# Performance work log

Measured on AMD Instinct MI355X. Metric: run time of the kernel, lower is better.

Reference implementation:

```python
import jax, jax.numpy as jnp
import numpy as np

HID = 512      # LSTM hidden per direction (1024 // 2)
EMB = 768      # BERT hidden size
NUM_TAG = 9
B, S = 64, 512


def setup_inputs() -> dict:
    key = jax.random.key(0)
    ks = jax.random.split(key, 12)
    g = lambda k, sh, sc: (jax.random.normal(k, sh, jnp.float32) * sc)
    return {
        "x": jax.random.normal(ks[0], (B, S, EMB), jnp.float32),
        "mask": jnp.ones((B, S), jnp.int32),
        "target_tag": jax.random.randint(ks[1], (B, S), 0, NUM_TAG, jnp.int32),
        "w_ih_f": g(ks[2], (4 * HID, EMB), 0.02),
        "w_hh_f": g(ks[3], (4 * HID, HID), 0.02),
        "b_f": jnp.zeros((4 * HID,), jnp.float32),
        "w_ih_b": g(ks[4], (4 * HID, EMB), 0.02),
        "w_hh_b": g(ks[5], (4 * HID, HID), 0.02),
        "b_b": jnp.zeros((4 * HID,), jnp.float32),
        "w_out": g(ks[6], (NUM_TAG, 2 * HID), 0.02),
        "b_out": jnp.zeros((NUM_TAG,), jnp.float32),
        "start_trans": g(ks[7], (NUM_TAG,), 0.1),
        "end_trans": g(ks[8], (NUM_TAG,), 0.1),
        "trans": g(ks[9], (NUM_TAG, NUM_TAG), 0.1),
    }


def _lstm_dir(x, w_ih, w_hh, b, reverse):
    # x: [B,S,E] -> outputs [S,B,H]; PyTorch gate order i,f,g,o
    xp = jnp.einsum('bse,ge->sbg', x, w_ih) + b  # precompute input proj [S,B,4H]
    if reverse:
        xp = xp[::-1]
    Bq = x.shape[0]
    def step(carry, xt):
        h, c = carry
        pre = xt + h @ w_hh.T
        i, f, g_, o = jnp.split(pre, 4, axis=-1)
        c = jax.nn.sigmoid(f) * c + jax.nn.sigmoid(i) * jnp.tanh(g_)
        h = jax.nn.sigmoid(o) * jnp.tanh(c)
        return (h, c), h
    init = (jnp.zeros((Bq, HID), x.dtype), jnp.zeros((Bq, HID), x.dtype))
    _, hs = jax.lax.scan(step, init, xp)
    if reverse:
        hs = hs[::-1]
    return hs


def _crf_nll_token_mean(emis, tags, m, start_trans, end_trans, trans):
    # emis: [S,B,T] time-major; tags: [S,B] int; m: [S,B] float (mask)
    Sq, Bq, T = emis.shape
    bidx = jnp.arange(Bq)
    # ---- numerator: score of the gold path ----
    num = start_trans[tags[0]] + emis[0, bidx, tags[0]]
    trans_steps = trans[tags[:-1], tags[1:]]                                   # [S-1,B]
    emit_steps = jnp.take_along_axis(emis[1:], tags[1:, :, None], axis=2)[..., 0]
    num = num + ((trans_steps + emit_steps) * m[1:]).sum(0)
    last_idx = m.sum(0).astype(jnp.int32) - 1                                   # [B]
    num = num + end_trans[tags[last_idx, bidx]]
    # ---- denominator: forward algorithm (log-sum-exp recursion) ----
    alpha0 = start_trans + emis[0]                                              # [B,T]
    def step(alpha, em):
        emis_t, m_t = em
        nxt = jax.nn.logsumexp(alpha[:, :, None] + trans[None] + emis_t[:, None, :], axis=1)
        return jnp.where(m_t[:, None] > 0, nxt, alpha), None
    alpha, _ = jax.lax.scan(step, alpha0, (emis[1:], m[1:]))
    den = jax.nn.logsumexp(alpha + end_trans, axis=1)
    llh = num - den
    return -(llh.sum() / m.sum())  # reduction='token_mean', negated (model loss)


def reference(x, mask, target_tag, w_ih_f, w_hh_f, b_f, w_ih_b, w_hh_b, b_b,
              w_out, b_out, start_trans, end_trans, trans):
    hf = _lstm_dir(x, w_ih_f, w_hh_f, b_f, reverse=False)   # [S,B,H]
    hb = _lstm_dir(x, w_ih_b, w_hh_b, b_b, reverse=True)    # [S,B,H]
    h = jnp.concatenate([hf, hb], axis=-1)                  # [S,B,2H]
    emis = jnp.einsum('sbh,th->sbt', h, w_out) + b_out      # [S,B,T] (dropout=identity in eval)
    tags = target_tag.T                                     # [S,B]
    m = mask.T.astype(emis.dtype)                           # [S,B]
    return _crf_nll_token_mean(emis, tags, m, start_trans, end_trans, trans)
```

## Files before the change

kernel.cpp:

```cpp
#include <hip/hip_runtime.h>
#include <cstdint>
#include <cstddef>

#define SS   512
#define BB   64
#define EMBD 768
#define HIDN 512
#define G4   2048
#define NTAG 9

typedef __attribute__((ext_vector_type(8))) __bf16 bf16x8;
typedef __attribute__((ext_vector_type(4))) float  f32x4;
typedef unsigned long long u64;

union HCast { f32x4 f; bf16x8 h; };

__device__ inline void load_h16_bypass(const void* base, f32x4* f) {
  asm volatile(
    "global_load_dwordx4 %0, %16, off sc0 sc1\n\t"
    "global_load_dwordx4 %1, %16, off offset:64 sc0 sc1\n\t"
    "global_load_dwordx4 %2, %16, off offset:128 sc0 sc1\n\t"
    "global_load_dwordx4 %3, %16, off offset:192 sc0 sc1\n\t"
    "global_load_dwordx4 %4, %16, off offset:256 sc0 sc1\n\t"
    "global_load_dwordx4 %5, %16, off offset:320 sc0 sc1\n\t"
    "global_load_dwordx4 %6, %16, off offset:384 sc0 sc1\n\t"
    "global_load_dwordx4 %7, %16, off offset:448 sc0 sc1\n\t"
    "global_load_dwordx4 %8, %16, off offset:512 sc0 sc1\n\t"
    "global_load_dwordx4 %9, %16, off offset:576 sc0 sc1\n\t"
    "global_load_dwordx4 %10, %16, off offset:640 sc0 sc1\n\t"
    "global_load_dwordx4 %11, %16, off offset:704 sc0 sc1\n\t"
    "global_load_dwordx4 %12, %16, off offset:768 sc0 sc1\n\t"
    "global_load_dwordx4 %13, %16, off offset:832 sc0 sc1\n\t"
    "global_load_dwordx4 %14, %16, off offset:896 sc0 sc1\n\t"
    "global_load_dwordx4 %15, %16, off offset:960 sc0 sc1\n\t"
    "s_waitcnt vmcnt(0)"
    : "=&v"(f[0]), "=&v"(f[1]), "=&v"(f[2]), "=&v"(f[3]),
      "=&v"(f[4]), "=&v"(f[5]), "=&v"(f[6]), "=&v"(f[7]),
      "=&v"(f[8]), "=&v"(f[9]), "=&v"(f[10]), "=&v"(f[11]),
      "=&v"(f[12]), "=&v"(f[13]), "=&v"(f[14]), "=&v"(f[15])
    : "v"(base)
    : "memory");
}
__device__ inline void store_h8_bypass(void* p, u64 v) {
  asm volatile("global_store_dwordx2 %0, %1, off sc0 sc1" :: "v"(p), "v"(v) : "memory");
}
__device__ inline void store_i32_bypass(int* p, int v) {
  asm volatile("global_store_dword %0, %1, off sc0 sc1" :: "v"(p), "v"(v) : "memory");
}
__device__ inline int load_i32_bypass(const int* p) {
  int v;
  asm volatile("global_load_dword %0, %1, off sc0 sc1\n\ts_waitcnt vmcnt(0)"
               : "=v"(v) : "v"(p) : "memory");
  return v;
}

__global__ __launch_bounds__(256) void cvt_kernel(
    const float* __restrict__ src, __bf16* __restrict__ dst, int n8)
{
  int i = blockIdx.x * 256 + threadIdx.x;
  if (i >= n8) return;
  f32x4 a = *reinterpret_cast<const f32x4*>(src + 8 * (size_t)i);
  f32x4 b = *reinterpret_cast<const f32x4*>(src + 8 * (size_t)i + 4);
  bf16x8 o;
  o[0]=(__bf16)a[0]; o[1]=(__bf16)a[1]; o[2]=(__bf16)a[2]; o[3]=(__bf16)a[3];
  o[4]=(__bf16)b[0]; o[5]=(__bf16)b[1]; o[6]=(__bf16)b[2]; o[7]=(__bf16)b[3];
  *reinterpret_cast<bf16x8*>(dst + 8 * (size_t)i) = o;
}

__global__ __launch_bounds__(256, 2) void proj_kernel(
    const __bf16* __restrict__ xb, const __bf16* __restrict__ wfb,
    const __bf16* __restrict__ wbb, const float* __restrict__ bias_f,
    const float* __restrict__ bias_b, float* __restrict__ xp,
    int t0, int chunk)
{
  const int nb = blockIdx.x;
  const int tt = blockIdx.y;
  const int d  = blockIdx.z;
  const int s  = d ? (SS - 1 - (t0 + tt)) : (t0 + tt);
  const __bf16* __restrict__ wih = d ? wbb : wfb;
  const float*  __restrict__ bias = d ? bias_b : bias_f;

  const int t = threadIdx.x, wv = t >> 6, l = t & 63;
  const int quad = l >> 4, col = l & 15;

  const __bf16* brow[8];
  float bj[8];
  const int pbase = 128 * nb;
#pragma unroll
  for (int j = 0; j < 8; j++) {
    int p    = pbase + 16 * j + col;
    int gate = p & 3;
    int hc   = 16 * (p >> 6) + 4 * ((p >> 2) & 3) + ((p >> 4) & 3);
    int g    = gate * HIDN + hc;
    brow[j]  = wih + (size_t)g * EMBD + 8 * quad;
    bj[j]    = bias[g];
  }
  const __bf16* arow = xb + ((size_t)(16 * wv + col) * SS + s) * EMBD + 8 * quad;

  f32x4 acc[8];
#pragma unroll
  for (int j = 0; j < 8; j++) acc[j] = f32x4{0.f, 0.f, 0.f, 0.f};

  for (int kk = 0; kk < 24; kk++) {
    bf16x8 a = *reinterpret_cast<const bf16x8*>(arow + 32 * kk);
#pragma unroll
    for (int j = 0; j < 8; j++) {
      bf16x8 b = *reinterpret_cast<const bf16x8*>(brow[j] + 32 * kk);
      acc[j] = __builtin_amdgcn_mfma_f32_16x16x32_bf16(a, b, acc[j], 0, 0, 0);
    }
  }
  float* xpd = xp + (size_t)(d * chunk + tt) * (size_t)G4 * BB + 16 * wv + 4 * quad;
#pragma unroll
  for (int j = 0; j < 8; j++) {
    int p = pbase + 16 * j + col;
    f32x4 v = acc[j];
    v[0] += bj[j]; v[1] += bj[j]; v[2] += bj[j]; v[3] += bj[j];
    *reinterpret_cast<f32x4*>(xpd + (size_t)p * BB) = v;
  }
}

struct RecCtl {
  int prog[2][64];
  int pad[128];
};

struct RecParams {
  const float* xp;
  const float* whh_f;
  const float* whh_b;
  __bf16* hh;
  float*  cT;
  RecCtl* ctl;
  int     chunk;
};

__global__ __launch_bounds__(256, 1) void rec_kernel(RecParams p)
{
  const int wg   = blockIdx.x;
  const int d    = wg >> 5;
  const int sl   = wg & 31;
  const int t    = threadIdx.x;
  const int wv   = t >> 6;
  const int l    = t & 63;
  const int quad = l >> 4;
  const int col  = l & 15;
  const int hcl  = col >> 2;
  const int gate = col & 3;
  const int j4   = col & 3;

  const float* __restrict__ whh = d ? p.whh_b : p.whh_f;

  bf16x8 bfrag[4][16];
#pragma unroll
  for (int j = 0; j < 4; j++) {
    const int hcb = 16 * sl + 4 * hcl + j;
    const float* wr = whh + (size_t)(gate * HIDN + hcb) * HIDN + 8 * quad;
#pragma unroll
    for (int kk = 0; kk < 16; kk++) {
      f32x4 w0 = *reinterpret_cast<const f32x4*>(wr + 32 * kk);
      f32x4 w1 = *reinterpret_cast<const f32x4*>(wr + 32 * kk + 4);
      bf16x8 v;
      v[0] = (__bf16)w0[0]; v[1] = (__bf16)w0[1]; v[2] = (__bf16)w0[2]; v[3] = (__bf16)w0[3];
      v[4] = (__bf16)w1[0]; v[5] = (__bf16)w1[1]; v[6] = (__bf16)w1[2]; v[7] = (__bf16)w1[3];
      bfrag[j][kk] = v;
    }
  }

  const int bA = 16 * wv + col;
  const int bC = 16 * wv + 4 * quad + gate;
  const int hcs = 16 * sl + 4 * hcl;
  const size_t slotsz = (size_t)BB * HIDN;
  __bf16* hhd = p.hh + (size_t)d * (p.chunk + 1) * slotsz;
  const float* xpd = p.xp + (size_t)d * p.chunk * ((size_t)G4 * BB);

  float c[4];
#pragma unroll
  for (int j = 0; j < 4; j++)
    c[j] = p.cT[((size_t)d * HIDN + hcs + j) * BB + bC];

  f32x4 xpn[4];
#pragma unroll
  for (int j = 0; j < 4; j++)
    xpn[j] = *reinterpret_cast<const f32x4*>(
        xpd + (size_t)(64 * sl + 16 * j + col) * BB + 16 * wv + 4 * quad);

  int* prog = &p.ctl->prog[d][0];
  const int* myslot = prog + (l & 31);

  u64 hword = 0;
  for (int tt = 0; tt < p.chunk; tt++) {
    const char* hbase = (const char*)hhd + (size_t)tt * slotsz * 2
                      + (size_t)bA * (HIDN * 2) + quad * 16;
    f32x4 araw[16];
    load_h16_bypass(hbase, araw);
    bf16x8 afrag[16];
#pragma unroll
    for (int kk = 0; kk < 16; kk++) { HCast hc_; hc_.f = araw[kk]; afrag[kk] = hc_.h; }

    f32x4 acc[4][2];
#pragma unroll
    for (int j = 0; j < 4; j++) {
      acc[j][0] = xpn[j];
      acc[j][1] = f32x4{0.f, 0.f, 0.f, 0.f};
    }
#pragma unroll
    for (int kk = 0; kk < 16; kk += 2) {
#pragma unroll
      for (int j = 0; j < 4; j++) {
        acc[j][0] = __builtin_amdgcn_mfma_f32_16x16x32_bf16(afrag[kk],     bfrag[j][kk],     acc[j][0], 0, 0, 0);
        acc[j][1] = __builtin_amdgcn_mfma_f32_16x16x32_bf16(afrag[kk + 1], bfrag[j][kk + 1], acc[j][1], 0, 0, 0);
      }
    }

    hword = 0;
#pragma unroll
    for (int j = 0; j < 4; j++) {
      float v0 = acc[j][0][0] + acc[j][1][0];
      float v1 = acc[j][0][1] + acc[j][1][1];
      float v2 = acc[j][0][2] + acc[j][1][2];
      float v3 = acc[j][0][3] + acc[j][1][3];
      {
        float t0 = __shfl_xor(v1, 1); float t1 = __shfl_xor(v0, 1);
        float t2 = __shfl_xor(v3, 1); float t3 = __shfl_xor(v2, 1);
        if (j4 & 1) { v0 = t0; v2 = t2; } else { v1 = t1; v3 = t3; }
        float u0 = __shfl_xor(v2, 2); float u1 = __shfl_xor(v3, 2);
        float u2 = __shfl_xor(v0, 2); float u3 = __shfl_xor(v1, 2);
        if (j4 & 2) { v0 = u0; v1 = u1; } else { v2 = u2; v3 = u3; }
      }
      float ig = 1.f / (1.f + __expf(-v0));
      float fg = 1.f / (1.f + __expf(-v1));
      float gg = 1.f - 2.f / (__expf(2.f * v2) + 1.f);
      float og = 1.f / (1.f + __expf(-v3));
      c[j] = fg * c[j] + ig * gg;
      float hn = og * (1.f - 2.f / (__expf(2.f * c[j]) + 1.f));
      union { __bf16 b; unsigned short u; } cv; cv.b = (__bf16)hn;
      hword |= (u64)cv.u << (16 * j);
    }
    store_h8_bypass((char*)hhd + (size_t)(tt + 1) * slotsz * 2
                    + (size_t)bC * (HIDN * 2) + (size_t)hcs * 2, hword);

    if (tt + 1 < p.chunk) {
#pragma unroll
      for (int j = 0; j < 4; j++)
        xpn[j] = *reinterpret_cast<const f32x4*>(
            xpd + (size_t)(tt + 1) * ((size_t)G4 * BB)
            + (size_t)(64 * sl + 16 * j + col) * BB + 16 * wv + 4 * quad);
    }

    __builtin_amdgcn_s_waitcnt(0);
    __syncthreads();
    if (t == 0) store_i32_bypass(prog + sl, tt + 1);
    if (wv == 0) {
      const int tgt = tt + 1;
      while (true) {
        int v = load_i32_bypass(myslot);
        if (__ballot(v >= tgt) == ~0ull) break;
        __builtin_amdgcn_s_sleep(1);
      }
    }
    __syncthreads();
    __atomic_signal_fence(__ATOMIC_SEQ_CST);
  }

  store_h8_bypass((char*)hhd + (size_t)bC * (HIDN * 2) + (size_t)hcs * 2, hword);
#pragma unroll
  for (int j = 0; j < 4; j++)
    p.cT[((size_t)d * HIDN + hcs + j) * BB + bC] = c[j];
}

__global__ __launch_bounds__(256) void emis_kernel(
    const __bf16* __restrict__ hh, const float* __restrict__ w_out,
    float* __restrict__ emis_f, float* __restrict__ emis_b,
    int t0, int chunk)
{
  const int tt = blockIdx.x;
  const int d  = blockIdx.y;
  const int t  = threadIdx.x;
  const int b  = t & 63;
  const int grp = t >> 6;

  const __bf16* hp = hh + ((size_t)d * (chunk + 1) + tt + 1) * ((size_t)BB * HIDN)
                   + (size_t)b * HIDN;
  const float* w0 = w_out + (size_t)grp * (2 * HIDN) + d * HIDN;
  const float* w1 = w_out + (size_t)(grp + 4) * (2 * HIDN) + d * HIDN;
  const float* w2 = w_out + (size_t)8 * (2 * HIDN) + d * HIDN;

  float a0 = 0.f, a1 = 0.f, a2 = 0.f;
  for (int k = 0; k < HIDN; k += 8) {
    bf16x8 hv8 = *reinterpret_cast<const bf16x8*>(hp + k);
#pragma unroll
    for (int j = 0; j < 8; j++) {
      float hv = (float)hv8[j];
      a0 += hv * w0[k + j];
      a1 += hv * w1[k + j];
      a2 += hv * w2[k + j];
    }
  }
  const int sidx = (d == 0) ? (t0 + tt) : (SS - 1 - (t0 + tt));
  float* dst = d ? emis_b : emis_f;
  dst[((size_t)sidx * BB + b) * NTAG + grp]     = a0;
  dst[((size_t)sidx * BB + b) * NTAG + grp + 4] = a1;
  if (grp == 0) dst[((size_t)sidx * BB + b) * NTAG + 8] = a2;
}

__global__ __launch_bounds__(64) void crf_kernel(
    const float* __restrict__ emis_f, const float* __restrict__ emis_b,
    const float* __restrict__ b_out, const float* __restrict__ start_tr,
    const float* __restrict__ end_tr, const float* __restrict__ trans,
    const int* __restrict__ mask, const int* __restrict__ target,
    float* __restrict__ llh)
{
  const int b    = blockIdx.x;
  const int lane = threadIdx.x;

  auto E = [&](int s, int tg) -> float {
    size_t o = ((size_t)s * BB + b) * NTAG + tg;
    return emis_f[o] + emis_b[o] + b_out[tg];
  };

  float numpart = 0.f;
  int msum = 0;
  for (int s = lane; s < SS; s += 64) {
    int m = mask[b * SS + s];
    msum += m;
    if (s >= 1 && m > 0) {
      int tp = target[b * SS + s - 1];
      int tc = target[b * SS + s];
      numpart += trans[tp * NTAG + tc] + E(s, tc);
    }
  }
#pragma unroll
  for (int off = 32; off > 0; off >>= 1) {
    numpart += __shfl_down(numpart, off, 64);
    msum    += __shfl_down(msum, off, 64);
  }

  const int tc = lane;
  const bool act = (tc < NTAG);
  float trc[NTAG] = {0.f};
  float alpha = 0.f;
  if (act) {
#pragma unroll
    for (int i = 0; i < NTAG; i++) trc[i] = trans[i * NTAG + tc];
    alpha = start_tr[tc] + E(0, tc);
  }
  for (int s = 1; s < SS; s++) {
    float e = act ? E(s, tc) : 0.f;
    float av[NTAG];
    float mx = -3.0e30f;
#pragma unroll
    for (int i = 0; i < NTAG; i++) {
      av[i] = __shfl(alpha, i, 64) + trc[i];
      mx = fmaxf(mx, av[i]);
    }
    float sum = 0.f;
#pragma unroll
    for (int i = 0; i < NTAG; i++) sum += __expf(av[i] - mx);
    float nxt = mx + __logf(sum) + e;
    if (act && mask[b * SS + s] > 0) alpha = nxt;
  }
  float fv = act ? (alpha + end_tr[tc]) : -3.0e30f;
  float q[NTAG];
  float mx2 = -3.0e30f;
#pragma unroll
  for (int i = 0; i < NTAG; i++) {
    q[i] = __shfl(fv, i, 64);
    mx2 = fmaxf(mx2, q[i]);
  }
  float s2 = 0.f;
#pragma unroll
  for (int i = 0; i < NTAG; i++) s2 += __expf(q[i] - mx2);
  float den = mx2 + __logf(s2);

  if (lane == 0) {
    int last = msum - 1;
    int tg0 = target[b * SS + 0];
    int tgl = target[b * SS + last];
    float num = start_tr[tg0] + E(0, tg0) + numpart + end_tr[tgl];
    llh[b] = num - den;
  }
}

__global__ __launch_bounds__(256) void fin_kernel(
    const float* __restrict__ llh, const int* __restrict__ mask,
    float* __restrict__ out)
{
  __shared__ float sf[256];
  __shared__ int   si[256];
  const int t = threadIdx.x;
  float a = (t < BB) ? llh[t] : 0.f;
  int m = 0;
  for (int i = t; i < BB * SS; i += 256) m += mask[i];
  sf[t] = a; si[t] = m;
  __syncthreads();
  for (int o = 128; o > 0; o >>= 1) {
    if (t < o) { sf[t] += sf[t + o]; si[t] += si[t + o]; }
    __syncthreads();
  }
  if (t == 0) out[0] = -(sf[0] / (float)si[0]);
}

extern "C" void kernel_launch(void* const* d_in, const int* in_sizes, int n_in,
                              void* d_out, int out_size, void* d_ws, size_t ws_size,
                              hipStream_t stream)
{
  const float* x     = (const float*)d_in[0];
  const int*   mask  = (const int*)d_in[1];
  const int*   targ  = (const int*)d_in[2];
  const float* wih_f = (const float*)d_in[3];
  const float* whh_f = (const float*)d_in[4];
  const float* b_f   = (const float*)d_in[5];
  const float* wih_b = (const float*)d_in[6];
  const float* whh_b = (const float*)d_in[7];
  const float* b_b   = (const float*)d_in[8];
  const float* w_out = (const float*)d_in[9];
  const float* b_out = (const float*)d_in[10];
  const float* st    = (const float*)d_in[11];
  const float* et    = (const float*)d_in[12];
  const float* tr    = (const float*)d_in[13];
  float* out = (float*)d_out;

  const size_t nxb   = (size_t)BB * SS * EMBD;
  const size_t nwb   = (size_t)G4 * EMBD;
  const size_t ctl_i = sizeof(RecCtl) / 4;
  const size_t fixed_f = (size_t)2 * SS * BB * NTAG + 64 + (size_t)2 * HIDN * BB
                       + ctl_i + nxb / 2 + nwb;
  int chunk = 1;
  for (int c = SS; c >= 1; c >>= 1) {
    size_t need = fixed_f * 4 + (size_t)c * 2 * G4 * BB * 4
                + (size_t)2 * (c + 1) * BB * HIDN * 2;
    if (need <= ws_size) { chunk = c; break; }
  }

  float* fp = (float*)d_ws;
  float* emis_f = fp; fp += (size_t)SS * BB * NTAG;
  float* emis_b = fp; fp += (size_t)SS * BB * NTAG;
  float* llh    = fp; fp += 64;
  float* cT     = fp; fp += (size_t)2 * HIDN * BB;
  RecCtl* ctl   = (RecCtl*)fp; fp += ctl_i;
  __bf16* xb16  = (__bf16*)fp; fp += nxb / 2;
  __bf16* wfb16 = (__bf16*)fp; fp += nwb / 2;
  __bf16* wbb16 = (__bf16*)fp; fp += nwb / 2;
  float* xp     = fp; fp += (size_t)chunk * 2 * G4 * BB;
  __bf16* hh    = (__bf16*)fp;

  {
    int n8 = (int)(nxb / 8);
    cvt_kernel<<<dim3((n8 + 255) / 256), 256, 0, stream>>>(x, xb16, n8);
    int w8 = (int)(nwb / 8);
    cvt_kernel<<<dim3((w8 + 255) / 256), 256, 0, stream>>>(wih_f, wfb16, w8);
    cvt_kernel<<<dim3((w8 + 255) / 256), 256, 0, stream>>>(wih_b, wbb16, w8);
  }

  const size_t slotsz = (size_t)BB * HIDN;
  hipMemsetAsync(cT, 0, (size_t)2 * HIDN * BB * sizeof(float), stream);
  hipMemsetAsync(hh, 0, slotsz * sizeof(__bf16), stream);
  hipMemsetAsync(hh + (size_t)(chunk + 1) * slotsz, 0, slotsz * sizeof(__bf16), stream);

  const int nch = SS / chunk;
  for (int c = 0; c < nch; c++) {
    const int t0 = c * chunk;
    hipMemsetAsync(ctl, 0, sizeof(RecCtl), stream);
    proj_kernel<<<dim3(16, chunk, 2), 256, 0, stream>>>(
        xb16, wfb16, wbb16, b_f, b_b, xp, t0, chunk);
    RecParams rp{xp, whh_f, whh_b, hh, cT, ctl, chunk};
    void* ka[] = {&rp};
    hipLaunchCooperativeKernel(rec_kernel, dim3(64), dim3(256), ka, 0, stream);
    emis_kernel<<<dim3(chunk, 2), 256, 0, stream>>>(
        hh, w_out, emis_f, emis_b, t0, chunk);
  }
  crf_kernel<<<dim3(64), 64, 0, stream>>>(emis_f, emis_b, b_out, st, et, tr, mask, targ, llh);
  fin_kernel<<<dim3(1), 256, 0, stream>>>(llh, mask, out);
}
```

Before: 5.001 ms.

## Replace block barrier with per-wave flags and retile input projection via LDS

The recurrence kernel drops its per-step block-wide barrier and global spin. Each wave now publishes its own progress flag and polls the flags of the producer groups, running the MFMAs for each 256-byte chunk of h as soon as that chunk is ready, so the recurrent matmul overlaps with waiting. The projection kernel is retiled to stage x and W_ih tiles in shared memory, computing 64x256 outputs per block, and x is converted to a time-major bf16 layout so each timestep's rows are contiguous. These changes add finer-grained memory-ordering logic whose correctness depends on the flag store being ordered after the h store.

```diff
diff --git a/kernel.cpp b/kernel.cpp
--- a/kernel.cpp
+++ b/kernel.cpp
@@ -15,31 +15,22 @@
 
 union HCast { f32x4 f; bf16x8 h; };
 
-__device__ inline void load_h16_bypass(const void* base, f32x4* f) {
+__device__ inline void load_h4_bypass(const void* base, f32x4* f) {
   asm volatile(
-    "global_load_dwordx4 %0, %16, off sc0 sc1\n\t"
-    "global_load_dwordx4 %1, %16, off offset:64 sc0 sc1\n\t"
-    "global_load_dwordx4 %2, %16, off offset:128 sc0 sc1\n\t"
-    "global_load_dwordx4 %3, %16, off offset:192 sc0 sc1\n\t"
-    "global_load_dwordx4 %4, %16, off offset:256 sc0 sc1\n\t"
-    "global_load_dwordx4 %5, %16, off offset:320 sc0 sc1\n\t"
-    "global_load_dwordx4 %6, %16, off offset:384 sc0 sc1\n\t"
-    "global_load_dwordx4 %7, %16, off offset:448 sc0 sc1\n\t"
-    "global_load_dwordx4 %8, %16, off offset:512 sc0 sc1\n\t"
-    "global_load_dwordx4 %9, %16, off offset:576 sc0 sc1\n\t"
-    "global_load_dwordx4 %10, %16, off offset:640 sc0 sc1\n\t"
-    "global_load_dwordx4 %11, %16, off offset:704 sc0 sc1\n\t"
-    "global_load_dwordx4 %12, %16, off offset:768 sc0 sc1\n\t"
-    "global_load_dwordx4 %13, %16, off offset:832 sc0 sc1\n\t"
-    "global_load_dwordx4 %14, %16, off offset:896 sc0 sc1\n\t"
-    "global_load_dwordx4 %15, %16, off offset:960 sc0 sc1\n\t"
+    "global_load_dwordx4 %0, %4, off sc0 sc1\n\t"
+    "global_load_dwordx4 %1, %4, off offset:64 sc0 sc1\n\t"
+    "global_load_dwordx4 %2, %4, off offset:128 sc0 sc1\n\t"
+    "global_load_dwordx4 %3, %4, off offset:192 sc0 sc1\n\t"
     "s_waitcnt vmcnt(0)"
-    : "=&v"(f[0]), "=&v"(f[1]), "=&v"(f[2]), "=&v"(f[3]),
-      "=&v"(f[4]), "=&v"(f[5]), "=&v"(f[6]), "=&v"(f[7]),
-      "=&v"(f[8]), "=&v"(f[9]), "=&v"(f[10]), "=&v"(f[11]),
-      "=&v"(f[12]), "=&v"(f[13]), "=&v"(f[14]), "=&v"(f[15])
-    : "v"(base)
-    : "memory");
+    : "=&v"(f[0]), "=&v"(f[1]), "=&v"(f[2]), "=&v"(f[3])
+    : "v"(base) : "memory");
+}
+__device__ inline void load_flags2(const int* p, int& a, int& b) {
+  asm volatile(
+    "global_load_dword %0, %2, off sc0 sc1\n\t"
+    "global_load_dword %1, %2, off offset:256 sc0 sc1\n\t"
+    "s_waitcnt vmcnt(0)"
+    : "=&v"(a), "=&v"(b) : "v"(p) : "memory");
 }
 __device__ inline void store_h8_bypass(void* p, u64 v) {
   asm volatile("global_store_dwordx2 %0, %1, off sc0 sc1" :: "v"(p), "v"(v) : "memory");
@@ -47,11 +38,8 @@
 __device__ inline void store_i32_bypass(int* p, int v) {
   asm volatile("global_store_dword %0, %1, off sc0 sc1" :: "v"(p), "v"(v) : "memory");
 }
-__device__ inline int load_i32_bypass(const int* p) {
-  int v;
-  asm volatile("global_load_dword %0, %1, off sc0 sc1\n\ts_waitcnt vmcnt(0)"
-               : "=v"(v) : "v"(p) : "memory");
-  return v;
+__device__ inline void wait_vm0() {
+  asm volatile("s_waitcnt vmcnt(0)" ::: "memory");
 }
 
 __global__ __launch_bounds__(256) void cvt_kernel(
@@ -67,6 +55,23 @@
   *reinterpret_cast<bf16x8*>(dst + 8 * (size_t)i) = o;
 }
 
+__global__ __launch_bounds__(256) void cvt_x_kernel(
+    const float* __restrict__ x, __bf16* __restrict__ xb)
+{
+  int i = blockIdx.x * 256 + threadIdx.x;
+  int e8 = i % 96;
+  int r  = i / 96;
+  int b  = r & 63;
+  int s  = r >> 6;
+  const float* src = x + ((size_t)b * SS + s) * EMBD + e8 * 8;
+  f32x4 a = *reinterpret_cast<const f32x4*>(src);
+  f32x4 c = *reinterpret_cast<const f32x4*>(src + 4);
+  bf16x8 o;
+  o[0]=(__bf16)a[0]; o[1]=(__bf16)a[1]; o[2]=(__bf16)a[2]; o[3]=(__bf16)a[3];
+  o[4]=(__bf16)c[0]; o[5]=(__bf16)c[1]; o[6]=(__bf16)c[2]; o[7]=(__bf16)c[3];
+  *reinterpret_cast<bf16x8*>(xb + ((size_t)s * BB + b) * EMBD + e8 * 8) = o;
+}
+
 __global__ __launch_bounds__(256, 2) void proj_kernel(
     const __bf16* __restrict__ xb, const __bf16* __restrict__ wfb,
     const __bf16* __restrict__ wbb, const float* __restrict__ bias_f,
@@ -77,51 +82,85 @@
   const int tt = blockIdx.y;
   const int d  = blockIdx.z;
   const int s  = d ? (SS - 1 - (t0 + tt)) : (t0 + tt);
-  const __bf16* __restrict__ wih = d ? wbb : wfb;
+  const __bf16* __restrict__ wih  = d ? wbb : wfb;
   const float*  __restrict__ bias = d ? bias_b : bias_f;
 
-  const int t = threadIdx.x, wv = t >> 6, l = t & 63;
-  const int quad = l >> 4, col = l & 15;
-
-  const __bf16* brow[8];
-  float bj[8];
-  const int pbase = 128 * nb;
-#pragma unroll
-  for (int j = 0; j < 8; j++) {
-    int p    = pbase + 16 * j + col;
-    int gate = p & 3;
-    int hc   = 16 * (p >> 6) + 4 * ((p >> 2) & 3) + ((p >> 4) & 3);
-    int g    = gate * HIDN + hc;
-    brow[j]  = wih + (size_t)g * EMBD + 8 * quad;
-    bj[j]    = bias[g];
-  }
-  const __bf16* arow = xb + ((size_t)(16 * wv + col) * SS + s) * EMBD + 8 * quad;
-
-  f32x4 acc[8];
-#pragma unroll
-  for (int j = 0; j < 8; j++) acc[j] = f32x4{0.f, 0.f, 0.f, 0.f};
-
-  for (int kk = 0; kk < 24; kk++) {
-    bf16x8 a = *reinterpret_cast<const bf16x8*>(arow + 32 * kk);
-#pragma unroll
-    for (int j = 0; j < 8; j++) {
-      bf16x8 b = *reinterpret_cast<const bf16x8*>(brow[j] + 32 * kk);
-      acc[j] = __builtin_amdgcn_mfma_f32_16x16x32_bf16(a, b, acc[j], 0, 0, 0);
-    }
-  }
-  float* xpd = xp + (size_t)(d * chunk + tt) * (size_t)G4 * BB + 16 * wv + 4 * quad;
-#pragma unroll
-  for (int j = 0; j < 8; j++) {
-    int p = pbase + 16 * j + col;
-    f32x4 v = acc[j];
-    v[0] += bj[j]; v[1] += bj[j]; v[2] += bj[j]; v[3] += bj[j];
-    *reinterpret_cast<f32x4*>(xpd + (size_t)p * BB) = v;
-  }
+  __shared__ __bf16 Asm[64 * 80];
+  __shared__ __bf16 Bsm[256 * 80];
+
+  const int t    = threadIdx.x;
+  const int wv   = t >> 6;
+  const int l    = t & 63;
+  const int quad = l >> 4;
+  const int col  = l & 15;
+
+  float bj[4];
+#pragma unroll
+  for (int j = 0; j < 4; j++) {
+    int p = 256 * nb + 64 * wv + 16 * j + col;
+    int g = (p & 3) * HIDN + 16 * (p >> 6) + 4 * ((p >> 2) & 3) + ((p >> 4) & 3);
+    bj[j] = bias[g];
+  }
+
+  f32x4 acc[4][4];
+#pragma unroll
+  for (int i = 0; i < 4; i++)
+#pragma unroll
+    for (int j = 0; j < 4; j++) acc[i][j] = f32x4{0.f, 0.f, 0.f, 0.f};
+
+  const int r32 = t >> 3;
+  const int m8  = t & 7;
+  const __bf16* xrow_base = xb + (size_t)s * BB * EMBD;
+
+  for (int kc = 0; kc < 12; kc++) {
+    const int k0 = kc * 64;
+    __syncthreads();
+#pragma unroll
+    for (int rr = 0; rr < 2; rr++) {
+      int r = r32 + 32 * rr;
+      *reinterpret_cast<bf16x8*>(Asm + r * 80 + m8 * 8) =
+          *reinterpret_cast<const bf16x8*>(xrow_base + (size_t)r * EMBD + k0 + m8 * 8);
+    }
+#pragma unroll
+    for (int rr = 0; rr < 8; rr++) {
+      int r = r32 + 32 * rr;
+      int p = 256 * nb + r;
+      int g = (p & 3) * HIDN + 16 * (p >> 6) + 4 * ((p >> 2) & 3) + ((p >> 4) & 3);
+      *reinterpret_cast<bf16x8*>(Bsm + r * 80 + m8 * 8) =
+          *reinterpret_cast<const bf16x8*>(wih + (size_t)g * EMBD + k0 + m8 * 8);
+    }
+    __syncthreads();
+#pragma unroll
+    for (int kkk = 0; kkk < 2; kkk++) {
+      bf16x8 af[4], bf[4];
+#pragma unroll
+      for (int i = 0; i < 4; i++)
+        af[i] = *reinterpret_cast<const bf16x8*>(Asm + (16 * i + col) * 80 + kkk * 32 + quad * 8);
+#pragma unroll
+      for (int j = 0; j < 4; j++)
+        bf[j] = *reinterpret_cast<const bf16x8*>(Bsm + (64 * wv + 16 * j + col) * 80 + kkk * 32 + quad * 8);
+#pragma unroll
+      for (int i = 0; i < 4; i++)
+#pragma unroll
+        for (int j = 0; j < 4; j++)
+          acc[i][j] = __builtin_amdgcn_mfma_f32_16x16x32_bf16(af[i], bf[j], acc[i][j], 0, 0, 0);
+    }
+  }
+  float* xpd = xp + (size_t)(d * chunk + tt) * (size_t)G4 * BB;
+#pragma unroll
+  for (int i = 0; i < 4; i++)
+#pragma unroll
+    for (int j = 0; j < 4; j++) {
+      int p = 256 * nb + 64 * wv + 16 * j + col;
+      f32x4 v = acc[i][j];
+      v[0] += bj[j]; v[1] += bj[j]; v[2] += bj[j]; v[3] += bj[j];
+      *reinterpret_cast<f32x4*>(xpd + (size_t)p * BB + 16 * i + 4 * quad) = v;
+    }
 }
 
 struct RecCtl {
-  int prog[2][64];
-  int pad[128];
+  int prog[2][128];
+  int pad[64];
 };
 
 struct RecParams {
@@ -185,17 +224,13 @@
         xpd + (size_t)(64 * sl + 16 * j + col) * BB + 16 * wv + 4 * quad);
 
   int* prog = &p.ctl->prog[d][0];
-  const int* myslot = prog + (l & 31);
+  const int* myflag = prog + l;
+  int* ownflag = prog + sl * 4 + wv;
 
   u64 hword = 0;
   for (int tt = 0; tt < p.chunk; tt++) {
     const char* hbase = (const char*)hhd + (size_t)tt * slotsz * 2
                       + (size_t)bA * (HIDN * 2) + quad * 16;
-    f32x4 araw[16];
-    load_h16_bypass(hbase, araw);
-    bf16x8 afrag[16];
-#pragma unroll
-    for (int kk = 0; kk < 16; kk++) { HCast hc_; hc_.f = araw[kk]; afrag[kk] = hc_.h; }
 
     f32x4 acc[4][2];
 #pragma unroll
@@ -203,12 +238,37 @@
       acc[j][0] = xpn[j];
       acc[j][1] = f32x4{0.f, 0.f, 0.f, 0.f};
     }
-#pragma unroll
-    for (int kk = 0; kk < 16; kk += 2) {
-#pragma unroll
-      for (int j = 0; j < 4; j++) {
-        acc[j][0] = __builtin_amdgcn_mfma_f32_16x16x32_bf16(afrag[kk],     bfrag[j][kk],     acc[j][0], 0, 0, 0);
-        acc[j][1] = __builtin_amdgcn_mfma_f32_16x16x32_bf16(afrag[kk + 1], bfrag[j][kk + 1], acc[j][1], 0, 0, 0);
+
+    auto process_group = [&](int g) {
+      f32x4 ar[4];
+      load_h4_bypass(hbase + 256 * g, ar);
+#pragma unroll
+      for (int q = 0; q < 4; q++) {
+        HCast hc_; hc_.f = ar[q];
+        bf16x8 af = hc_.h;
+        const int kk = 4 * g + q;
+#pragma unroll
+        for (int j = 0; j < 4; j++)
+          acc[j][q & 1] = __builtin_amdgcn_mfma_f32_16x16x32_bf16(af, bfrag[j][kk], acc[j][q & 1], 0, 0, 0);
+      }
+    };
+
+    if (tt == 0) {
+      for (int g = 0; g < 4; g++) process_group(g);
+    } else {
+      int done = 0;
+      while (done < 4) {
+        int fa, fb;
+        load_flags2(myflag, fa, fb);
+        u64 ba = __ballot(fa >= tt);
+        u64 bb = __ballot(fb >= tt);
+        bool rdy[4] = { (ba & 0xffffffffull) == 0xffffffffull,
+                        (ba >> 32)          == 0xffffffffull,
+                        (bb & 0xffffffffull) == 0xffffffffull,
+                        (bb >> 32)          == 0xffffffffull };
+        bool prog_made = false;
+        while (done < 4 && rdy[done]) { process_group(done); done++; prog_made = true; }
+        if (done < 4 && !prog_made) __builtin_amdgcn_s_sleep(1);
       }
     }
 
@@ -238,6 +298,8 @@
     }
     store_h8_bypass((char*)hhd + (size_t)(tt + 1) * slotsz * 2
                     + (size_t)bC * (HIDN * 2) + (size_t)hcs * 2, hword);
+    wait_vm0();
+    if (l == 0) store_i32_bypass(ownflag, tt + 1);
 
     if (tt + 1 < p.chunk) {
 #pragma unroll
@@ -246,20 +308,6 @@
             xpd + (size_t)(tt + 1) * ((size_t)G4 * BB)
             + (size_t)(64 * sl + 16 * j + col) * BB + 16 * wv + 4 * quad);
     }
-
-    __builtin_amdgcn_s_waitcnt(0);
-    __syncthreads();
-    if (t == 0) store_i32_bypass(prog + sl, tt + 1);
-    if (wv == 0) {
-      const int tgt = tt + 1;
-      while (true) {
-        int v = load_i32_bypass(myslot);
-        if (__ballot(v >= tgt) == ~0ull) break;
-        __builtin_amdgcn_s_sleep(1);
-      }
-    }
-    __syncthreads();
-    __atomic_signal_fence(__ATOMIC_SEQ_CST);
   }
 
   store_h8_bypass((char*)hhd + (size_t)bC * (HIDN * 2) + (size_t)hcs * 2, hword);
@@ -445,8 +493,8 @@
   __bf16* hh    = (__bf16*)fp;
 
   {
-    int n8 = (int)(nxb / 8);
-    cvt_kernel<<<dim3((n8 + 255) / 256), 256, 0, stream>>>(x, xb16, n8);
+    int nx8 = (int)(nxb / 8);
+    cvt_x_kernel<<<dim3((nx8 + 255) / 256), 256, 0, stream>>>(x, xb16);
     int w8 = (int)(nwb / 8);
     cvt_kernel<<<dim3((w8 + 255) / 256), 256, 0, stream>>>(wih_f, wfb16, w8);
     cvt_kernel<<<dim3((w8 + 255) / 256), 256, 0, stream>>>(wih_b, wbb16, w8);
@@ -461,7 +509,7 @@
   for (int c = 0; c < nch; c++) {
     const int t0 = c * chunk;
     hipMemsetAsync(ctl, 0, sizeof(RecCtl), stream);
-    proj_kernel<<<dim3(16, chunk, 2), 256, 0, stream>>>(
+    proj_kernel<<<dim3(8, chunk, 2), 256, 0, stream>>>(
         xb16, wfb16, wbb16, b_f, b_b, xp, t0, chunk);
     RecParams rp{xp, whh_f, whh_b, hh, cT, ctl, chunk};
     void* ka[] = {&rp};
```

New measurement: 7.391 ms. 47.8% more time.
